# Kernel tuning notes

Hardware: AMD Instinct MI355X
Metric: run time of the kernel (lower is better)

The kernel has to match this reference:

```python
import jax, jax.numpy as jnp
import numpy as np

# DAG configuration (fixed, mirrors the networkx dG used at construction time)
B = 4096          # batch
N_INP = 4096      # genes
L0 = 512          # leaf GO terms, each mapped to G disjoint genes
G = 8             # genes per leaf term
H = 16            # module_neurons (uniform per-module hidden size)
FAN = 8           # children per internal module -> input size FAN*H = 128
L1, L2 = 64, 8    # internal level sizes; root has L2=8 children


def setup_inputs() -> dict:
    key = jax.random.key(0)
    ks = jax.random.split(key, 8)
    s = lambda *sh: 0.1
    x = jax.random.normal(ks[0], (B, N_INP), dtype=jnp.float32)
    # Gene (RestrictedLayer) effective weights: kernel*connections is one-hot,
    # so only kernel[gene_idx[m,j], j] survives -> store as [L0, G] + bias.
    Wg = jax.random.normal(ks[1], (L0, G), dtype=jnp.float32) * 0.1
    bg = jax.random.normal(ks[2], (L0, G), dtype=jnp.float32) * 0.1
    # Per-level module Dense kernels (sigmoid, no bias)
    W0 = jax.random.normal(ks[3], (L0, G, H), dtype=jnp.float32) * 0.1       # leaf terms: G -> H
    W1 = jax.random.normal(ks[4], (L1, FAN * H, H), dtype=jnp.float32) * 0.1  # 128 -> 16
    W2 = jax.random.normal(ks[5], (L2, FAN * H, H), dtype=jnp.float32) * 0.1  # 128 -> 16
    W3 = jax.random.normal(ks[6], (FAN * H, H), dtype=jnp.float32) * 0.1      # root: 128 -> 16
    Wf = jax.random.normal(ks[7], (H, 1), dtype=jnp.float32) * 0.1            # final linear, no bias
    return {"x": x, "Wg": Wg, "bg": bg, "W0": W0, "W1": W1, "W2": W2,
            "W3": W3, "Wf": Wf}


def reference(x, Wg, bg, W0, W1, W2, W3, Wf):
    b = x.shape[0]
    # Input gene layers (RestrictedLayer, linear activation):
    # leaf m owns contiguous genes [m*G, (m+1)*G) -> gather is a reshape.
    gene_out = x.reshape(b, L0, G) * Wg + bg                    # [B, L0, G]
    # Level 0 (leaf GO terms): Dense(G->H), sigmoid, no bias
    h0 = jax.nn.sigmoid(jnp.einsum('bmg,mgh->bmh', gene_out, W0))   # [B, L0, H]
    # Level 1: concat FAN children's H outputs -> Dense(FAN*H -> H), sigmoid
    h1 = jax.nn.sigmoid(jnp.einsum('bmk,mkh->bmh',
                                   h0.reshape(b, L1, FAN * H), W1))  # [B, L1, H]
    # Level 2
    h2 = jax.nn.sigmoid(jnp.einsum('bmk,mkh->bmh',
                                   h1.reshape(b, L2, FAN * H), W2))  # [B, L2, H]
    # Root 'GO:output'
    hr = jax.nn.sigmoid(h2.reshape(b, FAN * H) @ W3)                 # [B, H]
    # Final Dense(1), linear, no bias
    return hr @ Wf                                                   # [B, 1]
```

## Files before the change

### kernel.cpp

```cpp
#include <hip/hip_runtime.h>
#include <hip/hip_bf16.h>


#define TB 16
#define H1S 136

typedef __attribute__((ext_vector_type(8))) short short8;
typedef __attribute__((ext_vector_type(4))) float floatx4;

__device__ __forceinline__ float sigf(float v) {
    return __builtin_amdgcn_rcpf(1.0f + __expf(-v));
}
__device__ __forceinline__ unsigned int f2bf2(float lo, float hi) {
    __hip_bfloat162 p = __float22bfloat162_rn(make_float2(lo, hi));
    unsigned int u;
    __builtin_memcpy(&u, &p, 4);
    return u;
}
__device__ __forceinline__ unsigned short f2bf(float f) {
    __hip_bfloat16 b = __float2bfloat16(f);
    unsigned short u;
    __builtin_memcpy(&u, &b, 2);
    return u;
}

__global__ __launch_bounds__(256) void k_prep(
    const float* __restrict__ W1, const float* __restrict__ W2,
    const float* __restrict__ Wg, const float* __restrict__ bg,
    const float* __restrict__ W0,
    unsigned short* __restrict__ W1t, unsigned short* __restrict__ W2t,
    unsigned short* __restrict__ W0f, float* __restrict__ bias0g)
{
    __shared__ float wl[128 * 17];
    const int mb  = blockIdx.x;
    const int tid = threadIdx.x;
    if (mb < 72) {
        const float* src = (mb < 64) ? (W1 + (size_t)mb * 2048)
                                     : (W2 + (size_t)(mb - 64) * 2048);
        unsigned short* dst = (mb < 64) ? (W1t + (size_t)mb * 2048)
                                        : (W2t + (size_t)(mb - 64) * 2048);
#pragma unroll
        for (int i = 0; i < 8; ++i) {
            const int idx = tid + i * 256;
            wl[(idx >> 4) * 17 + (idx & 15)] = src[idx];
        }
        __syncthreads();
#pragma unroll
        for (int i = 0; i < 4; ++i) {
            const int u  = tid + i * 256;
            const int h  = u >> 6;
            const int k  = (u & 63) * 2;
            ((unsigned int*)dst)[u] = f2bf2(wl[k * 17 + h], wl[(k + 1) * 17 + h]);
        }
    } else {
        const int idx = mb - 72;
        const int sub = tid >> 6, l = tid & 63;
#pragma unroll
        for (int it = 0; it < 2; ++it) {
            const int m = idx * 8 + it * 4 + sub;
            uint4 v = make_uint4(0u, 0u, 0u, 0u);
            if (l < 16) {
                float p[8];
                float bsum = 0.f;
#pragma unroll
                for (int j = 0; j < 8; ++j) {
                    const float w = W0[(size_t)m * 128 + j * 16 + l];
                    p[j] = Wg[m * 8 + j] * w;
                    bsum = fmaf(bg[m * 8 + j], w, bsum);
                }
                v.x = f2bf2(p[0], p[1]);
                v.y = f2bf2(p[2], p[3]);
                v.z = f2bf2(p[4], p[5]);
                v.w = f2bf2(p[6], p[7]);
                bias0g[m * 16 + l] = bsum;
            }
            *(uint4*)(W0f + (size_t)m * 512 + l * 8) = v;
        }
    }
}

struct FragG { uint4 a0, a1, a2, a3; float4 b0, b1, b2, b3; };

__device__ __forceinline__ void load4(FragG& f, const unsigned short* w0fp,
                                      const float* bp, int g) {
    f.a0 = *(const uint4*)(w0fp + (size_t)(g * 4 + 0) * 512);
    f.a1 = *(const uint4*)(w0fp + (size_t)(g * 4 + 1) * 512);
    f.a2 = *(const uint4*)(w0fp + (size_t)(g * 4 + 2) * 512);
    f.a3 = *(const uint4*)(w0fp + (size_t)(g * 4 + 3) * 512);
    f.b0 = *(const float4*)(bp + (g * 4 + 0) * 16);
    f.b1 = *(const float4*)(bp + (g * 4 + 1) * 16);
    f.b2 = *(const float4*)(bp + (g * 4 + 2) * 16);
    f.b3 = *(const float4*)(bp + (g * 4 + 3) * 16);
}

__device__ __forceinline__ void comp4(const FragG& f, int g, int m0,
                                      const char* xrd, char* h0wr,
                                      int brow, int q) {
#pragma unroll
    for (int i = 0; i < 4; ++i) {
        const uint4  a4 = (i == 0) ? f.a0 : (i == 1) ? f.a1 : (i == 2) ? f.a2 : f.a3;
        const float4 b4 = (i == 0) ? f.b0 : (i == 1) ? f.b1 : (i == 2) ? f.b2 : f.b3;
        const int mloc = m0 + g * 4 + i;
        const short8 bv = *(const short8*)(xrd + ((mloc * 16) ^ ((brow & 7) << 4)));
        floatx4 acc = {b4.x, b4.y, b4.z, b4.w};
        acc = __builtin_amdgcn_mfma_f32_16x16x32_bf16(
                  __builtin_bit_cast(short8, a4), bv, acc, 0, 0, 0);
        *(uint2*)(h0wr + ((mloc * 32 + q * 8) ^ ((brow & 7) << 4))) =
            make_uint2(f2bf2(sigf(acc[0]), sigf(acc[1])),
                       f2bf2(sigf(acc[2]), sigf(acc[3])));
    }
}

__global__ __launch_bounds__(256, 3) void k_tree(
    const float* __restrict__ x,
    const unsigned short* __restrict__ W0f, const float* __restrict__ bias0g,
    const unsigned short* __restrict__ W1t, const unsigned short* __restrict__ W2t,
    float* __restrict__ h2ws)
{
    __shared__ __align__(16) unsigned short xs[16 * 512];
    __shared__ __align__(16) unsigned short h0s[16 * 1024];
    unsigned short* h1u = xs;

    const int tid  = threadIdx.x;
    const int s    = blockIdx.x & 7;
    const int b0   = (blockIdx.x >> 3) * TB;
    const int lane = tid & 63;
    const int wv   = tid >> 6;
    const int n    = lane & 15, q = lane >> 4;

    const float* xbase = x + (size_t)b0 * 4096 + s * 512;
    uint2 xp[8];
#pragma unroll
    for (int t = 0; t < 8; ++t) {
        const int i = tid + t * 256;
        const int r = i >> 7, c4 = i & 127;
        const float4 v = *(const float4*)(xbase + (size_t)r * 4096 + c4 * 4);
        xp[t] = make_uint2(f2bf2(v.x, v.y), f2bf2(v.z, v.w));
    }

    short8 w1r[2][4];
#pragma unroll
    for (int jj = 0; jj < 2; ++jj) {
        const unsigned short* w1m =
            W1t + ((size_t)(s * 8 + wv * 2 + jj) * 16 + n) * 128 + q * 8;
#pragma unroll
        for (int ks = 0; ks < 4; ++ks)
            w1r[jj][ks] = *(const short8*)(w1m + ks * 32);
    }
    short8 w2r[4];
    if (wv == 0) {
        const unsigned short* w2m = W2t + ((size_t)s * 16 + n) * 128 + q * 8;
#pragma unroll
        for (int ks = 0; ks < 4; ++ks) w2r[ks] = *(const short8*)(w2m + ks * 32);
    }

#pragma unroll
    for (int t = 0; t < 8; ++t) {
        const int i = tid + t * 256;
        const int r = i >> 7, c4 = i & 127;
        *(uint2*)((char*)xs + r * 1024 + ((c4 * 8) ^ ((r & 7) << 4))) = xp[t];
    }
    __syncthreads();

    {
        const int m0 = wv * 16;
        const unsigned short* w0fp = W0f + ((size_t)(s * 64 + m0) * 64 + lane) * 8;
        const float* bp = bias0g + (size_t)(s * 64 + m0) * 16 + q * 4;
        const int brow = lane & 15;
        const char* xrd = (const char*)xs + brow * 1024;
        char* h0wr = (char*)h0s + brow * 2048;
        FragG fA, fB;
        load4(fA, w0fp, bp, 0);
        load4(fB, w0fp, bp, 1);
        comp4(fA, 0, m0, xrd, h0wr, brow, q);
        load4(fA, w0fp, bp, 2);
        comp4(fB, 1, m0, xrd, h0wr, brow, q);
        load4(fB, w0fp, bp, 3);
        comp4(fA, 2, m0, xrd, h0wr, brow, q);
        comp4(fB, 3, m0, xrd, h0wr, brow, q);
    }
    __syncthreads();

    {
        char* const h0b = (char*)h0s;
        const int swn = (n & 7) << 4;
#pragma unroll
        for (int jj = 0; jj < 2; ++jj) {
            const int j = wv * 2 + jj;
            floatx4 acc = {0.f, 0.f, 0.f, 0.f};
#pragma unroll
            for (int ks = 0; ks < 4; ++ks) {
                const short8 av = *(const short8*)(h0b + n * 2048 +
                                   ((j * 256 + q * 16 + ks * 64) ^ swn));
                acc = __builtin_amdgcn_mfma_f32_16x16x32_bf16(av, w1r[jj][ks], acc, 0, 0, 0);
            }
#pragma unroll
            for (int r = 0; r < 4; ++r)
                h1u[(q * 4 + r) * H1S + j * 16 + n] = f2bf(sigf(acc[r]));
        }
    }
    __syncthreads();

    if (wv == 0) {
        const unsigned short* am = &h1u[n * H1S + q * 8];
        floatx4 acc = {0.f, 0.f, 0.f, 0.f};
#pragma unroll
        for (int ks = 0; ks < 4; ++ks) {
            const short8 av = *(const short8*)(am + ks * 32);
            acc = __builtin_amdgcn_mfma_f32_16x16x32_bf16(av, w2r[ks], acc, 0, 0, 0);
        }
#pragma unroll
        for (int r = 0; r < 4; ++r)
            h2ws[(size_t)(b0 + q * 4 + r) * 128 + s * 16 + n] = sigf(acc[r]);
    }
}

__global__ __launch_bounds__(256) void k_root(
    const float* __restrict__ h2ws, const float* __restrict__ W3,
    const float* __restrict__ Wf, float* __restrict__ out)
{
    __shared__ float w3s[2048];
    __shared__ float wfs[16];
    const int tid = threadIdx.x;
    *(float4*)&w3s[tid * 8]     = *(const float4*)(W3 + tid * 8);
    *(float4*)&w3s[tid * 8 + 4] = *(const float4*)(W3 + tid * 8 + 4);
    if (tid < 16) wfs[tid] = Wf[tid];
    __syncthreads();

    const int h = tid & 15;
    const int b = blockIdx.x * 16 + (tid >> 4);
    const float4* hp = (const float4*)(h2ws + (size_t)b * 128);
    float acc = 0.f;
#pragma unroll
    for (int k4 = 0; k4 < 32; ++k4) {
        const float4 hv = hp[k4];
        acc = fmaf(hv.x, w3s[(k4 * 4 + 0) * 16 + h], acc);
        acc = fmaf(hv.y, w3s[(k4 * 4 + 1) * 16 + h], acc);
        acc = fmaf(hv.z, w3s[(k4 * 4 + 2) * 16 + h], acc);
        acc = fmaf(hv.w, w3s[(k4 * 4 + 3) * 16 + h], acc);
    }
    float v = sigf(acc) * wfs[h];
    v += __shfl_down(v, 8, 16);
    v += __shfl_down(v, 4, 16);
    v += __shfl_down(v, 2, 16);
    v += __shfl_down(v, 1, 16);
    if (h == 0) out[b] = v;
}

extern "C" void kernel_launch(void* const* d_in, const int* in_sizes, int n_in,
                              void* d_out, int out_size, void* d_ws, size_t ws_size,
                              hipStream_t stream) {
    const float* x  = (const float*)d_in[0];
    const float* Wg = (const float*)d_in[1];
    const float* bg = (const float*)d_in[2];
    const float* W0 = (const float*)d_in[3];
    const float* W1 = (const float*)d_in[4];
    const float* W2 = (const float*)d_in[5];
    const float* W3 = (const float*)d_in[6];
    const float* Wf = (const float*)d_in[7];
    float* out = (float*)d_out;

    float* h2 = (float*)d_ws;
    unsigned short* W1t = (unsigned short*)((char*)d_ws + (size_t)2 * 1024 * 1024);
    unsigned short* W2t = W1t + (size_t)64 * 2048;
    unsigned short* W0f = (unsigned short*)((char*)d_ws + (size_t)2 * 1024 * 1024
                                                        + (size_t)512 * 1024);
    float* bias0g = (float*)((char*)d_ws + (size_t)3 * 1024 * 1024);

    k_prep<<<dim3(136), dim3(256), 0, stream>>>(W1, W2, Wg, bg, W0,
                                                W1t, W2t, W0f, bias0g);
    k_tree<<<dim3((4096 / TB) * 8), dim3(256), 0, stream>>>(
        x, W0f, bias0g, W1t, W2t, h2);
    k_root<<<dim3(4096 / 16), dim3(256), 0, stream>>>(h2, W3, Wf, out);
}
```

Before: 117.7 us.

## Fuse root layer into tree kernel via last-block atomic counter per batch tile

```diff
diff --git a/kernel.cpp b/kernel.cpp
--- a/kernel.cpp
+++ b/kernel.cpp
@@ -29,11 +29,13 @@
     const float* __restrict__ Wg, const float* __restrict__ bg,
     const float* __restrict__ W0,
     unsigned short* __restrict__ W1t, unsigned short* __restrict__ W2t,
-    unsigned short* __restrict__ W0f, float* __restrict__ bias0g)
+    unsigned short* __restrict__ W0f, float* __restrict__ bias0g,
+    int* __restrict__ cnt)
 {
     __shared__ float wl[128 * 17];
     const int mb  = blockIdx.x;
     const int tid = threadIdx.x;
+    if (mb == 0) cnt[tid] = 0;
     if (mb < 72) {
         const float* src = (mb < 64) ? (W1 + (size_t)mb * 2048)
                                      : (W2 + (size_t)(mb - 64) * 2048);
@@ -115,15 +117,18 @@
     const float* __restrict__ x,
     const unsigned short* __restrict__ W0f, const float* __restrict__ bias0g,
     const unsigned short* __restrict__ W1t, const unsigned short* __restrict__ W2t,
-    float* __restrict__ h2ws)
+    const float* __restrict__ W3, const float* __restrict__ Wf,
+    float* __restrict__ h2ws, int* __restrict__ cnt, float* __restrict__ out)
 {
     __shared__ __align__(16) unsigned short xs[16 * 512];
     __shared__ __align__(16) unsigned short h0s[16 * 1024];
+    __shared__ int lastflag;
     unsigned short* h1u = xs;
 
     const int tid  = threadIdx.x;
     const int s    = blockIdx.x & 7;
-    const int b0   = (blockIdx.x >> 3) * TB;
+    const int tile = blockIdx.x >> 3;
+    const int b0   = tile * TB;
     const int lane = tid & 63;
     const int wv   = tid >> 6;
     const int n    = lane & 15, q = lane >> 4;
@@ -211,40 +216,43 @@
         }
 #pragma unroll
         for (int r = 0; r < 4; ++r)
-            h2ws[(size_t)(b0 + q * 4 + r) * 128 + s * 16 + n] = sigf(acc[r]);
-    }
-}
-
-__global__ __launch_bounds__(256) void k_root(
-    const float* __restrict__ h2ws, const float* __restrict__ W3,
-    const float* __restrict__ Wf, float* __restrict__ out)
-{
-    __shared__ float w3s[2048];
-    __shared__ float wfs[16];
-    const int tid = threadIdx.x;
-    *(float4*)&w3s[tid * 8]     = *(const float4*)(W3 + tid * 8);
-    *(float4*)&w3s[tid * 8 + 4] = *(const float4*)(W3 + tid * 8 + 4);
-    if (tid < 16) wfs[tid] = Wf[tid];
-    __syncthreads();
-
-    const int h = tid & 15;
-    const int b = blockIdx.x * 16 + (tid >> 4);
-    const float4* hp = (const float4*)(h2ws + (size_t)b * 128);
-    float acc = 0.f;
-#pragma unroll
-    for (int k4 = 0; k4 < 32; ++k4) {
-        const float4 hv = hp[k4];
-        acc = fmaf(hv.x, w3s[(k4 * 4 + 0) * 16 + h], acc);
-        acc = fmaf(hv.y, w3s[(k4 * 4 + 1) * 16 + h], acc);
-        acc = fmaf(hv.z, w3s[(k4 * 4 + 2) * 16 + h], acc);
-        acc = fmaf(hv.w, w3s[(k4 * 4 + 3) * 16 + h], acc);
-    }
-    float v = sigf(acc) * wfs[h];
-    v += __shfl_down(v, 8, 16);
-    v += __shfl_down(v, 4, 16);
-    v += __shfl_down(v, 2, 16);
-    v += __shfl_down(v, 1, 16);
-    if (h == 0) out[b] = v;
+            __hip_atomic_store(&h2ws[(size_t)(b0 + q * 4 + r) * 128 + s * 16 + n],
+                               sigf(acc[r]), __ATOMIC_RELAXED,
+                               __HIP_MEMORY_SCOPE_AGENT);
+    }
+    __syncthreads();
+    if (tid == 0) {
+        asm volatile("" ::: "memory");
+        lastflag = (__hip_atomic_fetch_add(&cnt[tile], 1, __ATOMIC_RELAXED,
+                                           __HIP_MEMORY_SCOPE_AGENT) == 7);
+        asm volatile("" ::: "memory");
+    }
+    __syncthreads();
+
+    if (lastflag) {
+        float* w3s = (float*)xs;
+        float* wfs = (float*)xs + 2048;
+        *(float4*)&w3s[tid * 8]     = *(const float4*)(W3 + tid * 8);
+        *(float4*)&w3s[tid * 8 + 4] = *(const float4*)(W3 + tid * 8 + 4);
+        if (tid < 16) wfs[tid] = Wf[tid];
+        __syncthreads();
+        const int h = tid & 15;
+        const int b = b0 + (tid >> 4);
+        const float* hp = h2ws + (size_t)b * 128;
+        float acc = 0.f;
+#pragma unroll 8
+        for (int k = 0; k < 128; ++k) {
+            const float hv = __hip_atomic_load(&hp[k], __ATOMIC_RELAXED,
+                                               __HIP_MEMORY_SCOPE_AGENT);
+            acc = fmaf(hv, w3s[k * 16 + h], acc);
+        }
+        float v = sigf(acc) * wfs[h];
+        v += __shfl_down(v, 8, 16);
+        v += __shfl_down(v, 4, 16);
+        v += __shfl_down(v, 2, 16);
+        v += __shfl_down(v, 1, 16);
+        if (h == 0) out[b] = v;
+    }
 }
 
 extern "C" void kernel_launch(void* const* d_in, const int* in_sizes, int n_in,
@@ -266,10 +274,10 @@
     unsigned short* W0f = (unsigned short*)((char*)d_ws + (size_t)2 * 1024 * 1024
                                                         + (size_t)512 * 1024);
     float* bias0g = (float*)((char*)d_ws + (size_t)3 * 1024 * 1024);
+    int* cnt = (int*)((char*)d_ws + (size_t)3 * 1024 * 1024 + (size_t)64 * 1024);
 
     k_prep<<<dim3(136), dim3(256), 0, stream>>>(W1, W2, Wg, bg, W0,
-                                                W1t, W2t, W0f, bias0g);
+                                                W1t, W2t, W0f, bias0g, cnt);
     k_tree<<<dim3((4096 / TB) * 8), dim3(256), 0, stream>>>(
-        x, W0f, bias0g, W1t, W2t, h2);
-    k_root<<<dim3(4096 / 16), dim3(256), 0, stream>>>(h2, W3, Wf, out);
-}
+        x, W0f, bias0g, W1t, W2t, W3, Wf, h2, cnt, out);
+}
```

Result: slower. 129.3 us (+9.9%).

## Fuse root layer into tree kernel via per-slice partial sums and atomics

Applied to the files above, without the earlier changes.

```diff
diff --git a/kernel.cpp b/kernel.cpp
--- a/kernel.cpp
+++ b/kernel.cpp
@@ -29,11 +29,17 @@
     const float* __restrict__ Wg, const float* __restrict__ bg,
     const float* __restrict__ W0,
     unsigned short* __restrict__ W1t, unsigned short* __restrict__ W2t,
-    unsigned short* __restrict__ W0f, float* __restrict__ bias0g)
+    unsigned short* __restrict__ W0f, float* __restrict__ bias0g,
+    float* __restrict__ pbuf)
 {
     __shared__ float wl[128 * 17];
     const int mb  = blockIdx.x;
     const int tid = threadIdx.x;
+    {
+        const int u = mb * 256 + tid;
+        if (u < 16384)
+            *(float4*)(pbuf + (size_t)u * 4) = make_float4(0.f, 0.f, 0.f, 0.f);
+    }
     if (mb < 72) {
         const float* src = (mb < 64) ? (W1 + (size_t)mb * 2048)
                                      : (W2 + (size_t)(mb - 64) * 2048);
@@ -115,7 +121,7 @@
     const float* __restrict__ x,
     const unsigned short* __restrict__ W0f, const float* __restrict__ bias0g,
     const unsigned short* __restrict__ W1t, const unsigned short* __restrict__ W2t,
-    float* __restrict__ h2ws)
+    const float* __restrict__ W3, float* __restrict__ pbuf)
 {
     __shared__ __align__(16) unsigned short xs[16 * 512];
     __shared__ __align__(16) unsigned short h0s[16 * 1024];
@@ -202,6 +208,13 @@
     __syncthreads();
 
     if (wv == 0) {
+        float* h2l = (float*)((char*)xs + 8192);
+        float* w3l = (float*)((char*)xs + 12288);
+        {
+            const int nn = lane >> 2, h4 = (lane & 3) * 4;
+            *(float4*)&w3l[nn * 16 + h4] =
+                *(const float4*)(W3 + (size_t)(s * 16 + nn) * 16 + h4);
+        }
         const unsigned short* am = &h1u[n * H1S + q * 8];
         floatx4 acc = {0.f, 0.f, 0.f, 0.f};
 #pragma unroll
@@ -211,40 +224,52 @@
         }
 #pragma unroll
         for (int r = 0; r < 4; ++r)
-            h2ws[(size_t)(b0 + q * 4 + r) * 128 + s * 16 + n] = sigf(acc[r]);
-    }
-}
-
-__global__ __launch_bounds__(256) void k_root(
-    const float* __restrict__ h2ws, const float* __restrict__ W3,
-    const float* __restrict__ Wf, float* __restrict__ out)
+            h2l[(q * 4 + r) * 16 + n] = sigf(acc[r]);
+        __builtin_amdgcn_wave_barrier();
+        const int b = lane & 15;
+        float pacc[4] = {0.f, 0.f, 0.f, 0.f};
+#pragma unroll
+        for (int k = 0; k < 16; ++k) {
+            const float hv = h2l[b * 16 + k];
+#pragma unroll
+            for (int j = 0; j < 4; ++j)
+                pacc[j] = fmaf(hv, w3l[k * 16 + (q + 4 * j)], pacc[j]);
+        }
+#pragma unroll
+        for (int j = 0; j < 4; ++j)
+            atomicAdd(&pbuf[(size_t)(b0 + b) * 16 + q + 4 * j], pacc[j]);
+    }
+}
+
+__global__ __launch_bounds__(256) void k_final(
+    const float* __restrict__ pbuf, const float* __restrict__ Wf,
+    float* __restrict__ out)
 {
-    __shared__ float w3s[2048];
     __shared__ float wfs[16];
     const int tid = threadIdx.x;
-    *(float4*)&w3s[tid * 8]     = *(const float4*)(W3 + tid * 8);
-    *(float4*)&w3s[tid * 8 + 4] = *(const float4*)(W3 + tid * 8 + 4);
     if (tid < 16) wfs[tid] = Wf[tid];
     __syncthreads();
-
-    const int h = tid & 15;
-    const int b = blockIdx.x * 16 + (tid >> 4);
-    const float4* hp = (const float4*)(h2ws + (size_t)b * 128);
-    float acc = 0.f;
-#pragma unroll
-    for (int k4 = 0; k4 < 32; ++k4) {
-        const float4 hv = hp[k4];
-        acc = fmaf(hv.x, w3s[(k4 * 4 + 0) * 16 + h], acc);
-        acc = fmaf(hv.y, w3s[(k4 * 4 + 1) * 16 + h], acc);
-        acc = fmaf(hv.z, w3s[(k4 * 4 + 2) * 16 + h], acc);
-        acc = fmaf(hv.w, w3s[(k4 * 4 + 3) * 16 + h], acc);
-    }
-    float v = sigf(acc) * wfs[h];
-    v += __shfl_down(v, 8, 16);
-    v += __shfl_down(v, 4, 16);
-    v += __shfl_down(v, 2, 16);
-    v += __shfl_down(v, 1, 16);
-    if (h == 0) out[b] = v;
+    const int b = blockIdx.x * 256 + tid;
+    const float4* pp = (const float4*)(pbuf + (size_t)b * 16);
+    const float4 p0 = pp[0], p1 = pp[1], p2 = pp[2], p3 = pp[3];
+    float v = 0.f;
+    v = fmaf(sigf(p0.x), wfs[0],  v);
+    v = fmaf(sigf(p0.y), wfs[1],  v);
+    v = fmaf(sigf(p0.z), wfs[2],  v);
+    v = fmaf(sigf(p0.w), wfs[3],  v);
+    v = fmaf(sigf(p1.x), wfs[4],  v);
+    v = fmaf(sigf(p1.y), wfs[5],  v);
+    v = fmaf(sigf(p1.z), wfs[6],  v);
+    v = fmaf(sigf(p1.w), wfs[7],  v);
+    v = fmaf(sigf(p2.x), wfs[8],  v);
+    v = fmaf(sigf(p2.y), wfs[9],  v);
+    v = fmaf(sigf(p2.z), wfs[10], v);
+    v = fmaf(sigf(p2.w), wfs[11], v);
+    v = fmaf(sigf(p3.x), wfs[12], v);
+    v = fmaf(sigf(p3.y), wfs[13], v);
+    v = fmaf(sigf(p3.z), wfs[14], v);
+    v = fmaf(sigf(p3.w), wfs[15], v);
+    out[b] = v;
 }
 
 extern "C" void kernel_launch(void* const* d_in, const int* in_sizes, int n_in,
@@ -260,7 +285,7 @@
     const float* Wf = (const float*)d_in[7];
     float* out = (float*)d_out;
 
-    float* h2 = (float*)d_ws;
+    float* pbuf = (float*)d_ws;
     unsigned short* W1t = (unsigned short*)((char*)d_ws + (size_t)2 * 1024 * 1024);
     unsigned short* W2t = W1t + (size_t)64 * 2048;
     unsigned short* W0f = (unsigned short*)((char*)d_ws + (size_t)2 * 1024 * 1024
@@ -268,8 +293,8 @@
     float* bias0g = (float*)((char*)d_ws + (size_t)3 * 1024 * 1024);
 
     k_prep<<<dim3(136), dim3(256), 0, stream>>>(W1, W2, Wg, bg, W0,
-                                                W1t, W2t, W0f, bias0g);
+                                                W1t, W2t, W0f, bias0g, pbuf);
     k_tree<<<dim3((4096 / TB) * 8), dim3(256), 0, stream>>>(
-        x, W0f, bias0g, W1t, W2t, h2);
-    k_root<<<dim3(4096 / 16), dim3(256), 0, stream>>>(h2, W3, Wf, out);
-}
+        x, W0f, bias0g, W1t, W2t, W3, pbuf);
+    k_final<<<dim3(4096 / 256), dim3(256), 0, stream>>>(pbuf, Wf, out);
+}
```

After: 119.9 us. No clear change (+1.8%).

## Process two batch tiles per block and prefetch second tile's x during compute

Applied to the files above, without the earlier changes.

```diff
diff --git a/kernel.cpp b/kernel.cpp
--- a/kernel.cpp
+++ b/kernel.cpp
@@ -111,6 +111,62 @@
     }
 }
 
+__device__ __forceinline__ void phaseA(int s, int lane, int wv, int q,
+    const unsigned short* __restrict__ W0f, const float* __restrict__ bias0g,
+    const char* xsb, char* h0b)
+{
+    const int m0 = wv * 16;
+    const unsigned short* w0fp = W0f + ((size_t)(s * 64 + m0) * 64 + lane) * 8;
+    const float* bp = bias0g + (size_t)(s * 64 + m0) * 16 + q * 4;
+    const int brow = lane & 15;
+    const char* xrd = xsb + brow * 1024;
+    char* h0wr = h0b + brow * 2048;
+    FragG fA, fB;
+    load4(fA, w0fp, bp, 0);
+    load4(fB, w0fp, bp, 1);
+    comp4(fA, 0, m0, xrd, h0wr, brow, q);
+    load4(fA, w0fp, bp, 2);
+    comp4(fB, 1, m0, xrd, h0wr, brow, q);
+    load4(fB, w0fp, bp, 3);
+    comp4(fA, 2, m0, xrd, h0wr, brow, q);
+    comp4(fB, 3, m0, xrd, h0wr, brow, q);
+}
+
+__device__ __forceinline__ void phaseB(int n, int q, int wv,
+    const short8 (&w1r)[2][4], const char* h0b, unsigned short* h1u)
+{
+    const int swn = (n & 7) << 4;
+#pragma unroll
+    for (int jj = 0; jj < 2; ++jj) {
+        const int j = wv * 2 + jj;
+        floatx4 acc = {0.f, 0.f, 0.f, 0.f};
+#pragma unroll
+        for (int ks = 0; ks < 4; ++ks) {
+            const short8 av = *(const short8*)(h0b + n * 2048 +
+                               ((j * 256 + q * 16 + ks * 64) ^ swn));
+            acc = __builtin_amdgcn_mfma_f32_16x16x32_bf16(av, w1r[jj][ks], acc, 0, 0, 0);
+        }
+#pragma unroll
+        for (int r = 0; r < 4; ++r)
+            h1u[(q * 4 + r) * H1S + j * 16 + n] = f2bf(sigf(acc[r]));
+    }
+}
+
+__device__ __forceinline__ void phaseC(int n, int q, int s, int b0,
+    const short8 (&w2r)[4], const unsigned short* h1u, float* __restrict__ h2ws)
+{
+    const unsigned short* am = &h1u[n * H1S + q * 8];
+    floatx4 acc = {0.f, 0.f, 0.f, 0.f};
+#pragma unroll
+    for (int ks = 0; ks < 4; ++ks) {
+        const short8 av = *(const short8*)(am + ks * 32);
+        acc = __builtin_amdgcn_mfma_f32_16x16x32_bf16(av, w2r[ks], acc, 0, 0, 0);
+    }
+#pragma unroll
+    for (int r = 0; r < 4; ++r)
+        h2ws[(size_t)(b0 + q * 4 + r) * 128 + s * 16 + n] = sigf(acc[r]);
+}
+
 __global__ __launch_bounds__(256, 3) void k_tree(
     const float* __restrict__ x,
     const unsigned short* __restrict__ W0f, const float* __restrict__ bias0g,
@@ -123,19 +179,22 @@
 
     const int tid  = threadIdx.x;
     const int s    = blockIdx.x & 7;
-    const int b0   = (blockIdx.x >> 3) * TB;
+    const int b0   = (blockIdx.x >> 3) * (2 * TB);
+    const int b1   = b0 + TB;
     const int lane = tid & 63;
     const int wv   = tid >> 6;
     const int n    = lane & 15, q = lane >> 4;
-
-    const float* xbase = x + (size_t)b0 * 4096 + s * 512;
-    uint2 xp[8];
+    char* const xsb = (char*)xs;
+    char* const h0b = (char*)h0s;
+
+    const float* xbase0 = x + (size_t)b0 * 4096 + s * 512;
+    uint2 xpA[8];
 #pragma unroll
     for (int t = 0; t < 8; ++t) {
         const int i = tid + t * 256;
         const int r = i >> 7, c4 = i & 127;
-        const float4 v = *(const float4*)(xbase + (size_t)r * 4096 + c4 * 4);
-        xp[t] = make_uint2(f2bf2(v.x, v.y), f2bf2(v.z, v.w));
+        const float4 v = *(const float4*)(xbase0 + (size_t)r * 4096 + c4 * 4);
+        xpA[t] = make_uint2(f2bf2(v.x, v.y), f2bf2(v.z, v.w));
     }
 
     short8 w1r[2][4];
@@ -158,61 +217,40 @@
     for (int t = 0; t < 8; ++t) {
         const int i = tid + t * 256;
         const int r = i >> 7, c4 = i & 127;
-        *(uint2*)((char*)xs + r * 1024 + ((c4 * 8) ^ ((r & 7) << 4))) = xp[t];
-    }
-    __syncthreads();
-
-    {
-        const int m0 = wv * 16;
-        const unsigned short* w0fp = W0f + ((size_t)(s * 64 + m0) * 64 + lane) * 8;
-        const float* bp = bias0g + (size_t)(s * 64 + m0) * 16 + q * 4;
-        const int brow = lane & 15;
-        const char* xrd = (const char*)xs + brow * 1024;
-        char* h0wr = (char*)h0s + brow * 2048;
-        FragG fA, fB;
-        load4(fA, w0fp, bp, 0);
-        load4(fB, w0fp, bp, 1);
-        comp4(fA, 0, m0, xrd, h0wr, brow, q);
-        load4(fA, w0fp, bp, 2);
-        comp4(fB, 1, m0, xrd, h0wr, brow, q);
-        load4(fB, w0fp, bp, 3);
-        comp4(fA, 2, m0, xrd, h0wr, brow, q);
-        comp4(fB, 3, m0, xrd, h0wr, brow, q);
-    }
-    __syncthreads();
-
-    {
-        char* const h0b = (char*)h0s;
-        const int swn = (n & 7) << 4;
-#pragma unroll
-        for (int jj = 0; jj < 2; ++jj) {
-            const int j = wv * 2 + jj;
-            floatx4 acc = {0.f, 0.f, 0.f, 0.f};
-#pragma unroll
-            for (int ks = 0; ks < 4; ++ks) {
-                const short8 av = *(const short8*)(h0b + n * 2048 +
-                                   ((j * 256 + q * 16 + ks * 64) ^ swn));
-                acc = __builtin_amdgcn_mfma_f32_16x16x32_bf16(av, w1r[jj][ks], acc, 0, 0, 0);
-            }
-#pragma unroll
-            for (int r = 0; r < 4; ++r)
-                h1u[(q * 4 + r) * H1S + j * 16 + n] = f2bf(sigf(acc[r]));
-        }
-    }
-    __syncthreads();
-
-    if (wv == 0) {
-        const unsigned short* am = &h1u[n * H1S + q * 8];
-        floatx4 acc = {0.f, 0.f, 0.f, 0.f};
-#pragma unroll
-        for (int ks = 0; ks < 4; ++ks) {
-            const short8 av = *(const short8*)(am + ks * 32);
-            acc = __builtin_amdgcn_mfma_f32_16x16x32_bf16(av, w2r[ks], acc, 0, 0, 0);
-        }
-#pragma unroll
-        for (int r = 0; r < 4; ++r)
-            h2ws[(size_t)(b0 + q * 4 + r) * 128 + s * 16 + n] = sigf(acc[r]);
-    }
+        *(uint2*)(xsb + r * 1024 + ((c4 * 8) ^ ((r & 7) << 4))) = xpA[t];
+    }
+    __syncthreads();
+
+    const float* xbase1 = x + (size_t)b1 * 4096 + s * 512;
+    float4 xrB[8];
+#pragma unroll
+    for (int t = 0; t < 8; ++t) {
+        const int i = tid + t * 256;
+        const int r = i >> 7, c4 = i & 127;
+        xrB[t] = *(const float4*)(xbase1 + (size_t)r * 4096 + c4 * 4);
+    }
+
+    phaseA(s, lane, wv, q, W0f, bias0g, xsb, h0b);
+    __syncthreads();
+    phaseB(n, q, wv, w1r, h0b, h1u);
+    __syncthreads();
+    if (wv == 0) phaseC(n, q, s, b0, w2r, h1u, h2ws);
+    __syncthreads();
+
+#pragma unroll
+    for (int t = 0; t < 8; ++t) {
+        const int i = tid + t * 256;
+        const int r = i >> 7, c4 = i & 127;
+        *(uint2*)(xsb + r * 1024 + ((c4 * 8) ^ ((r & 7) << 4))) =
+            make_uint2(f2bf2(xrB[t].x, xrB[t].y), f2bf2(xrB[t].z, xrB[t].w));
+    }
+    __syncthreads();
+
+    phaseA(s, lane, wv, q, W0f, bias0g, xsb, h0b);
+    __syncthreads();
+    phaseB(n, q, wv, w1r, h0b, h1u);
+    __syncthreads();
+    if (wv == 0) phaseC(n, q, s, b1, w2r, h1u, h2ws);
 }
 
 __global__ __launch_bounds__(256) void k_root(
@@ -269,7 +307,7 @@
 
     k_prep<<<dim3(136), dim3(256), 0, stream>>>(W1, W2, Wg, bg, W0,
                                                 W1t, W2t, W0f, bias0g);
-    k_tree<<<dim3((4096 / TB) * 8), dim3(256), 0, stream>>>(
+    k_tree<<<dim3((4096 / TB / 2) * 8), dim3(256), 0, stream>>>(
         x, W0f, bias0g, W1t, W2t, h2);
     k_root<<<dim3(4096 / 16), dim3(256), 0, stream>>>(h2, W3, Wf, out);
 }
```

Measured after the change: 135.1 us. 14.7% more time.
